# Kernel tuning notes

Hardware: AMD Instinct MI355X
Metric: run time of the kernel (lower is better)

The kernel has to match this reference:

```python
import jax, jax.numpy as jnp
import numpy as np

N = 262144
H = 256
POS_L, DIR_L = 10, 4


def _encode(x, L):
    # classic NeRF sinusoidal encoding with identity: [N,3] -> [N, 3 + 6*L]
    f = 2.0 ** jnp.arange(L, dtype=x.dtype)          # [L]
    xf = x[:, :, None] * f                            # [N,3,L]
    n = x.shape[0]
    return jnp.concatenate([x, jnp.sin(xf).reshape(n, -1), jnp.cos(xf).reshape(n, -1)], axis=1)


def setup_inputs() -> dict:
    key = jax.random.key(0)
    ks = iter(jax.random.split(key, 32))
    inp = {
        "pos": jax.random.normal(next(ks), (N, 3), jnp.float32),
        "dir": jax.random.normal(next(ks), (N, 3), jnp.float32),
        "pixel_width": jax.random.uniform(next(ks), (N, 1), dtype=jnp.float32),
        "t_start": jax.random.uniform(next(ks), (N, 1), dtype=jnp.float32),
        "t_end": jax.random.uniform(next(ks), (N, 1), dtype=jnp.float32),
    }
    pe_dim = 3 + 6 * POS_L   # 63
    de_dim = 3 + 6 * DIR_L   # 27
    dims = {
        "w00": (pe_dim, H), "w01": (H, H), "w02": (H, H), "w03": (H, H),
        "w10": (H + pe_dim, H), "w11": (H, H), "w12": (H, H), "w13": (H, H),
        "cw0": (H + de_dim, H // 2), "cw1": (H // 2, 4),
    }
    for name, (i, o) in dims.items():
        inp[name] = jax.random.normal(next(ks), (i, o), jnp.float32) * (1.0 / np.sqrt(i))
        inp[name.replace("w", "b", 1)] = jnp.zeros((o,), jnp.float32)
    return inp


def _nerf(pos, dir, w00, b00, w01, b01, w02, b02, w03, b03,
          w10, b10, w11, b11, w12, b12, w13, b13, cw0, cb0, cw1, cb1):
    pe = _encode(pos, POS_L)   # [N,63]
    de = _encode(dir, DIR_L)   # [N,27]
    r = jax.nn.relu
    # segment 0 (4 linears, ReLU between all, plus inter-segment ReLU)
    z = r(pe @ w00 + b00)
    z = r(z @ w01 + b01)
    z = r(z @ w02 + b02)
    z = r(z @ w03 + b03)
    # segment 1: positional encoding re-concatenated (skip connection)
    z = jnp.concatenate([z, pe], axis=1)              # [N,319]
    z = r(z @ w10 + b10)
    z = r(z @ w11 + b11)
    z = r(z @ w12 + b12)
    z = z @ w13 + b13                                 # no activation after last segment
    # color head: direction encoding concatenated (delayed_direction=True)
    h = r(jnp.concatenate([z, de], axis=1) @ cw0 + cb0)   # [N,128]
    out = h @ cw1 + cb1                                    # [N,4] (rgb + density, delayed_density=True)
    d = out[:, -1]
    density = jnp.where(d > 8.0, d, jax.nn.softplus(d))    # Softplus(threshold=8)
    rgb = jax.nn.sigmoid(out[:, :3])
    return density, rgb


def reference(pos, dir, pixel_width, t_start, t_end,
              w00, b00, w01, b01, w02, b02, w03, b03,
              w10, b10, w11, b11, w12, b12, w13, b13,
              cw0, cb0, cw1, cb1):
    # pixel_width / t_start / t_end are consumed only by mip-style encoders; the
    # classic sinusoidal encoder used here ignores them (kept for signature parity).
    return _nerf(pos, dir, w00, b00, w01, b01, w02, b02, w03, b03,
                 w10, b10, w11, b11, w12, b12, w13, b13, cw0, cb0, cw1, cb1)
```

## Files before the change

kernel.cpp:

```cpp
#include <hip/hip_runtime.h>
#include <hip/hip_bf16.h>
#include <math.h>

typedef unsigned short u16;
typedef unsigned int   u32;
typedef __bf16 bf16x8 __attribute__((ext_vector_type(8)));
typedef float  f32x4  __attribute__((ext_vector_type(4)));

#define NRAYS 262144
#define RPB   128
#define NBLK  (NRAYS / RPB)

enum : int { PO0=0, PO1=16384, PO2=81920, PO3=147456, PO4=212992,
             PO5=294912, PO6=360448, PO7=425984, PO8=491520, PO9=528384 };
#define TOTAL_PACK_ELEMS 530432

__device__ __forceinline__ u16 f2bf(float x) {
  return (u16)((__float_as_uint(x) + 0x8000u) >> 16);
}

struct PackArgs {
  const float* src[10];
  int K[10]; int N[10]; int l2mt[10]; int cstart[11];
};

__global__ __launch_bounds__(256) void pack_w(PackArgs a, u16* __restrict__ dst)
{
  int e = blockIdx.x * 256 + threadIdx.x;
  if (e >= TOTAL_PACK_ELEMS) return;
  int chunk = e >> 9;
  int li = 0;
  #pragma unroll
  for (int t = 1; t < 10; ++t) li += (chunk >= a.cstart[t]) ? 1 : 0;
  int lc = chunk - a.cstart[li];
  int ks = lc >> a.l2mt[li];
  int mt = lc - (ks << a.l2mt[li]);
  int lane = (e >> 3) & 63, j = e & 7;
  int k = ks * 32 + ((lane >> 4) << 3) + j;
  int n = mt * 16 + (lane & 15);
  float v = 0.f;
  if (k < a.K[li] && n < a.N[li]) v = a.src[li][(size_t)k * a.N[li] + n];
  u32 u = __float_as_uint(v);
  dst[e] = (u16)((u + 0x7FFFu + ((u >> 16) & 1u)) >> 16);
}

template<int MT_W>
__device__ __forceinline__ void binit(f32x4 acc[MT_W][4],
    const float* __restrict__ bias, int chbase, int lane)
{
  const int q = lane >> 4;
  #pragma unroll
  for (int mt = 0; mt < MT_W; ++mt) {
    float4 bv = *(const float4*)(bias + chbase + mt * 16 + q * 4);
    #pragma unroll
    for (int nt = 0; nt < 4; ++nt)
      acc[mt][nt] = (f32x4){bv.x, bv.y, bv.z, bv.w};
  }
}

template<int MT_W, int NSTEPS, int MT_TOTAL, int STRIDE>
__device__ __forceinline__ void gseg(f32x4 acc[MT_W][4],
    const u16* __restrict__ zb, int rhb, int cbase8,
    const u16* __restrict__ wl, int mt0, int ksbase, int lane)
{
  const int q = lane >> 4, llo = lane & 15;
  #pragma unroll
  for (int ks = 0; ks < NSTEPS; ++ks) {
    int c8s = ((cbase8 + ks * 4 + q) ^ (llo & 7));
    const u16* bp = zb + (rhb + llo) * STRIDE + c8s * 8;
    bf16x8 b[4];
    #pragma unroll
    for (int nt = 0; nt < 4; ++nt)
      b[nt] = *(const bf16x8*)(bp + nt * 16 * STRIDE);
    const u16* wp = wl + ((ksbase + ks) * MT_TOTAL + mt0) * 512 + lane * 8;
    bf16x8 a[MT_W];
    #pragma unroll
    for (int mt = 0; mt < MT_W; ++mt)
      a[mt] = *(const bf16x8*)(wp + mt * 512);
    #pragma unroll
    for (int mt = 0; mt < MT_W; ++mt)
      #pragma unroll
      for (int nt = 0; nt < 4; ++nt)
        acc[mt][nt] = __builtin_amdgcn_mfma_f32_16x16x32_bf16(a[mt], b[nt], acc[mt][nt], 0, 0, 0);
  }
}

template<int MT_W, bool RELU>
__device__ __forceinline__ void zstore(f32x4 acc[MT_W][4],
    int chbase, int rhb, u16* dst, int lane)
{
  const int llo = lane & 15, q = lane >> 4;
  #pragma unroll
  for (int mt = 0; mt < MT_W; ++mt) {
    int ch = chbase + mt * 16 + q * 4;
    int off0 = (((ch >> 3) ^ (llo & 7)) << 3) + (ch & 7);
    #pragma unroll
    for (int nt = 0; nt < 4; ++nt) {
      f32x4 v = acc[mt][nt];
      float x0 = v.x, x1 = v.y, x2 = v.z, x3 = v.w;
      if (RELU) { x0 = fmaxf(x0, 0.f); x1 = fmaxf(x1, 0.f);
                  x2 = fmaxf(x2, 0.f); x3 = fmaxf(x3, 0.f); }
      u32 a0 = __float_as_uint(x0) + 0x8000u;
      u32 a1 = __float_as_uint(x1) + 0x8000u;
      u32 a2 = __float_as_uint(x2) + 0x8000u;
      u32 a3 = __float_as_uint(x3) + 0x8000u;
      uint2 pk;
      pk.x = __builtin_amdgcn_perm(a1, a0, 0x07060302u);
      pk.y = __builtin_amdgcn_perm(a3, a2, 0x07060302u);
      *(uint2*)(dst + (rhb + nt * 16 + llo) * 256 + off0) = pk;
    }
  }
}

__device__ __forceinline__ void wr_pe(u16* peb, int r, int c, u16 v) {
  peb[r * 64 + (((c >> 3) ^ (r & 7)) << 3) + (c & 7)] = v;
}

__global__ __launch_bounds__(512, 4) void nerf_fused(
    const float* __restrict__ pos,  const float* __restrict__ dirv,
    const float* __restrict__ b00,  const float* __restrict__ b01,
    const float* __restrict__ b02,  const float* __restrict__ b03,
    const float* __restrict__ b10,  const float* __restrict__ b11,
    const float* __restrict__ b12,  const float* __restrict__ b13,
    const float* __restrict__ cb0,  const float* __restrict__ cb1,
    const u16* __restrict__ W, float* __restrict__ out)
{
  __shared__ __align__(16) u16 zb[RPB * 256];
  __shared__ __align__(16) u16 peb[RPB * 64];
  float* xyzf = (float*)zb;

  const int tid = threadIdx.x;
  const int rb  = blockIdx.x * RPB;
  const int lane = tid & 63, wid = tid >> 6;

  if (tid < 384) {
    int r = tid / 3, c = tid - r * 3;
    xyzf[r * 4 + c] = pos[(size_t)(rb + r) * 3 + c];
  }
  __syncthreads();

  #pragma unroll
  for (int i = tid; i < RPB * 30; i += 512) {
    int r = i / 30, t = i - r * 30;
    int j = t / 10, l = t - j * 10;
    float x = xyzf[r * 4 + j] * (float)(1 << l);
    wr_pe(peb, r, 3 + t,  f2bf(__sinf(x)));
    wr_pe(peb, r, 33 + t, f2bf(__cosf(x)));
  }
  {
    int r = tid >> 2, c = tid & 3;
    u16 v = 0; int col = 63;
    if (c < 3) { col = c; v = f2bf(xyzf[r * 4 + c]); }
    wr_pe(peb, r, col, v);
  }
  __syncthreads();

  f32x4 acc[4][4];
  const int mt0 = (wid & 3) * 4;
  const int chb = mt0 * 16;
  const int rh  = (wid >> 2) * 64;

  binit<4>(acc, b00, chb, lane);
  gseg<4, 2, 16, 64>(acc, peb, rh, 0, W + PO0, mt0, 0, lane);
  __syncthreads();
  zstore<4, true>(acc, chb, rh, zb, lane);
  __syncthreads();
  binit<4>(acc, b01, chb, lane);
  gseg<4, 8, 16, 256>(acc, zb, rh, 0, W + PO1, mt0, 0, lane);
  __syncthreads();
  zstore<4, true>(acc, chb, rh, zb, lane);
  __syncthreads();
  binit<4>(acc, b02, chb, lane);
  gseg<4, 8, 16, 256>(acc, zb, rh, 0, W + PO2, mt0, 0, lane);
  __syncthreads();
  zstore<4, true>(acc, chb, rh, zb, lane);
  __syncthreads();
  binit<4>(acc, b03, chb, lane);
  gseg<4, 8, 16, 256>(acc, zb, rh, 0, W + PO3, mt0, 0, lane);
  __syncthreads();
  zstore<4, true>(acc, chb, rh, zb, lane);
  __syncthreads();
  binit<4>(acc, b10, chb, lane);
  gseg<4, 8, 16, 256>(acc, zb, rh, 0, W + PO4, mt0, 0, lane);
  gseg<4, 2, 16, 64>(acc, peb, rh, 0, W + PO4, mt0, 8, lane);
  __syncthreads();
  zstore<4, true>(acc, chb, rh, zb, lane);
  #pragma unroll
  for (int i = tid; i < RPB * 16; i += 512) {
    int r = i >> 4, t = i & 15;
    if (t < 12) {
      int j = t >> 2, l = t & 3;
      float x = dirv[(size_t)(rb + r) * 3 + j] * (float)(1 << l);
      wr_pe(peb, r, 32 + 3 + t,  f2bf(__sinf(x)));
      wr_pe(peb, r, 32 + 15 + t, f2bf(__cosf(x)));
    } else {
      wr_pe(peb, r, 32 + 15 + t, 0);
    }
  }
  {
    int r = tid >> 2, c = tid & 3;
    u16 v = 0; int col = 31;
    if (c < 3) { col = c; v = f2bf(dirv[(size_t)(rb + r) * 3 + c]); }
    wr_pe(peb, r, 32 + col, v);
  }
  __syncthreads();
  binit<4>(acc, b11, chb, lane);
  gseg<4, 8, 16, 256>(acc, zb, rh, 0, W + PO5, mt0, 0, lane);
  __syncthreads();
  zstore<4, true>(acc, chb, rh, zb, lane);
  __syncthreads();
  binit<4>(acc, b12, chb, lane);
  gseg<4, 8, 16, 256>(acc, zb, rh, 0, W + PO6, mt0, 0, lane);
  __syncthreads();
  zstore<4, true>(acc, chb, rh, zb, lane);
  __syncthreads();
  binit<4>(acc, b13, chb, lane);
  gseg<4, 8, 16, 256>(acc, zb, rh, 0, W + PO7, mt0, 0, lane);
  __syncthreads();
  zstore<4, false>(acc, chb, rh, zb, lane);
  __syncthreads();
  {
    f32x4 acc8[2][4];
    const int m8 = (wid & 3) * 2;
    binit<2>(acc8, cb0, m8 * 16, lane);
    gseg<2, 8, 8, 256>(acc8, zb, rh, 0, W + PO8, m8, 0, lane);
    gseg<2, 1, 8, 64>(acc8, peb, rh, 4, W + PO8, m8, 8, lane);
    __syncthreads();
    zstore<2, true>(acc8, m8 * 16, rh, zb, lane);
    __syncthreads();
  }
  {
    const u16* W9 = W + PO9;
    const int q = lane >> 4, llo = lane & 15;
    const int r = wid * 16 + llo;
    f32x4 c9 = (f32x4){0.f, 0.f, 0.f, 0.f};
    #pragma unroll
    for (int ks = 0; ks < 4; ++ks) {
      int c8s = ((ks * 4 + q) ^ (llo & 7));
      bf16x8 b = *(const bf16x8*)(zb + r * 256 + c8s * 8);
      bf16x8 a = *(const bf16x8*)(W9 + ks * 512 + lane * 8);
      c9 = __builtin_amdgcn_mfma_f32_16x16x32_bf16(a, b, c9, 0, 0, 0);
    }
    if (q == 0) {
      int ray = rb + r;
      float o0 = c9.x + cb1[0];
      float o1 = c9.y + cb1[1];
      float o2 = c9.z + cb1[2];
      float dv = c9.w + cb1[3];
      out[ray] = (dv > 8.f) ? dv : log1pf(__expf(dv));
      float* rgb = out + NRAYS + (size_t)ray * 3;
      rgb[0] = 1.f / (1.f + __expf(-o0));
      rgb[1] = 1.f / (1.f + __expf(-o1));
      rgb[2] = 1.f / (1.f + __expf(-o2));
    }
  }
}

extern "C" void kernel_launch(void* const* d_in, const int* in_sizes, int n_in,
                              void* d_out, int out_size, void* d_ws, size_t ws_size,
                              hipStream_t stream)
{
  (void)in_sizes; (void)n_in; (void)out_size; (void)ws_size;
  const float* pos  = (const float*)d_in[0];
  const float* dirv = (const float*)d_in[1];
  PackArgs pa;
  const int widx[10] = {5, 7, 9, 11, 13, 15, 17, 19, 21, 23};
  const int K[10]    = {63, 256, 256, 256, 319, 256, 256, 256, 283, 128};
  const int Nn[10]   = {256, 256, 256, 256, 256, 256, 256, 256, 128, 4};
  const int L2MT[10] = {4, 4, 4, 4, 4, 4, 4, 4, 3, 0};
  const int CS[11]   = {0, 32, 160, 288, 416, 576, 704, 832, 960, 1032, 1036};
  for (int i = 0; i < 10; ++i) {
    pa.src[i] = (const float*)d_in[widx[i]];
    pa.K[i] = K[i]; pa.N[i] = Nn[i]; pa.l2mt[i] = L2MT[i];
  }
  for (int i = 0; i < 11; ++i) pa.cstart[i] = CS[i];

  u16* wp = (u16*)d_ws;
  hipLaunchKernelGGL(pack_w, dim3(TOTAL_PACK_ELEMS / 256), dim3(256), 0, stream, pa, wp);

  hipLaunchKernelGGL(nerf_fused, dim3(NBLK), dim3(512), 0, stream,
      pos, dirv,
      (const float*)d_in[6],  (const float*)d_in[8],
      (const float*)d_in[10], (const float*)d_in[12],
      (const float*)d_in[14], (const float*)d_in[16],
      (const float*)d_in[18], (const float*)d_in[20],
      (const float*)d_in[22], (const float*)d_in[24],
      wp, (float*)d_out);
}
```

Baseline: 391.3 us.

## Halve rays per block and stage direction encoding in a dedicated LDS buffer

```diff
diff --git a/kernel.cpp b/kernel.cpp
--- a/kernel.cpp
+++ b/kernel.cpp
@@ -8,7 +8,7 @@
 typedef float  f32x4  __attribute__((ext_vector_type(4)));
 
 #define NRAYS 262144
-#define RPB   128
+#define RPB   64
 #define NBLK  (NRAYS / RPB)
 
 enum : int { PO0=0, PO1=16384, PO2=81920, PO3=147456, PO4=212992,
@@ -44,8 +44,8 @@
   dst[e] = (u16)((u + 0x7FFFu + ((u >> 16) & 1u)) >> 16);
 }
 
-template<int MT_W>
-__device__ __forceinline__ void binit(f32x4 acc[MT_W][4],
+template<int MT_W, int NT>
+__device__ __forceinline__ void binit(f32x4 acc[MT_W][NT],
     const float* __restrict__ bias, int chbase, int lane)
 {
   const int q = lane >> 4;
@@ -53,24 +53,24 @@
   for (int mt = 0; mt < MT_W; ++mt) {
     float4 bv = *(const float4*)(bias + chbase + mt * 16 + q * 4);
     #pragma unroll
-    for (int nt = 0; nt < 4; ++nt)
+    for (int nt = 0; nt < NT; ++nt)
       acc[mt][nt] = (f32x4){bv.x, bv.y, bv.z, bv.w};
   }
 }
 
-template<int MT_W, int NSTEPS, int MT_TOTAL, int STRIDE>
-__device__ __forceinline__ void gseg(f32x4 acc[MT_W][4],
+template<int MT_W, int NT, int NSTEPS, int MT_TOTAL, int STRIDE, bool SWZ>
+__device__ __forceinline__ void gseg(f32x4 acc[MT_W][NT],
     const u16* __restrict__ zb, int rhb, int cbase8,
     const u16* __restrict__ wl, int mt0, int ksbase, int lane)
 {
   const int q = lane >> 4, llo = lane & 15;
   #pragma unroll
   for (int ks = 0; ks < NSTEPS; ++ks) {
-    int c8s = ((cbase8 + ks * 4 + q) ^ (llo & 7));
+    int c8s = (cbase8 + ks * 4 + q) ^ (SWZ ? (llo & 7) : 0);
     const u16* bp = zb + (rhb + llo) * STRIDE + c8s * 8;
-    bf16x8 b[4];
-    #pragma unroll
-    for (int nt = 0; nt < 4; ++nt)
+    bf16x8 b[NT];
+    #pragma unroll
+    for (int nt = 0; nt < NT; ++nt)
       b[nt] = *(const bf16x8*)(bp + nt * 16 * STRIDE);
     const u16* wp = wl + ((ksbase + ks) * MT_TOTAL + mt0) * 512 + lane * 8;
     bf16x8 a[MT_W];
@@ -80,13 +80,13 @@
     #pragma unroll
     for (int mt = 0; mt < MT_W; ++mt)
       #pragma unroll
-      for (int nt = 0; nt < 4; ++nt)
+      for (int nt = 0; nt < NT; ++nt)
         acc[mt][nt] = __builtin_amdgcn_mfma_f32_16x16x32_bf16(a[mt], b[nt], acc[mt][nt], 0, 0, 0);
   }
 }
 
-template<int MT_W, bool RELU>
-__device__ __forceinline__ void zstore(f32x4 acc[MT_W][4],
+template<int MT_W, int NT, bool RELU>
+__device__ __forceinline__ void zstore(f32x4 acc[MT_W][NT],
     int chbase, int rhb, u16* dst, int lane)
 {
   const int llo = lane & 15, q = lane >> 4;
@@ -95,7 +95,7 @@
     int ch = chbase + mt * 16 + q * 4;
     int off0 = (((ch >> 3) ^ (llo & 7)) << 3) + (ch & 7);
     #pragma unroll
-    for (int nt = 0; nt < 4; ++nt) {
+    for (int nt = 0; nt < NT; ++nt) {
       f32x4 v = acc[mt][nt];
       float x0 = v.x, x1 = v.y, x2 = v.z, x3 = v.w;
       if (RELU) { x0 = fmaxf(x0, 0.f); x1 = fmaxf(x1, 0.f);
@@ -127,15 +127,19 @@
 {
   __shared__ __align__(16) u16 zb[RPB * 256];
   __shared__ __align__(16) u16 peb[RPB * 64];
+  __shared__ __align__(16) u16 deb[RPB * 32];
   float* xyzf = (float*)zb;
 
   const int tid = threadIdx.x;
   const int rb  = blockIdx.x * RPB;
   const int lane = tid & 63, wid = tid >> 6;
 
-  if (tid < 384) {
+  if (tid < 192) {
     int r = tid / 3, c = tid - r * 3;
-    xyzf[r * 4 + c] = pos[(size_t)(rb + r) * 3 + c];
+    xyzf[r * 8 + c] = pos[(size_t)(rb + r) * 3 + c];
+  } else if (tid < 384) {
+    int t = tid - 192, r = t / 3, c = t - r * 3;
+    xyzf[r * 8 + 4 + c] = dirv[(size_t)(rb + r) * 3 + c];
   }
   __syncthreads();
 
@@ -143,93 +147,88 @@
   for (int i = tid; i < RPB * 30; i += 512) {
     int r = i / 30, t = i - r * 30;
     int j = t / 10, l = t - j * 10;
-    float x = xyzf[r * 4 + j] * (float)(1 << l);
+    float x = xyzf[r * 8 + j] * (float)(1 << l);
     wr_pe(peb, r, 3 + t,  f2bf(__sinf(x)));
     wr_pe(peb, r, 33 + t, f2bf(__cosf(x)));
   }
-  {
+  if (tid < 256) {
     int r = tid >> 2, c = tid & 3;
     u16 v = 0; int col = 63;
-    if (c < 3) { col = c; v = f2bf(xyzf[r * 4 + c]); }
+    if (c < 3) { col = c; v = f2bf(xyzf[r * 8 + c]); }
     wr_pe(peb, r, col, v);
   }
-  __syncthreads();
-
-  f32x4 acc[4][4];
+  #pragma unroll
+  for (int i = tid; i < RPB * 12; i += 512) {
+    int r = i / 12, t = i - r * 12;
+    int j = t >> 2, l = t & 3;
+    float x = xyzf[r * 8 + 4 + j] * (float)(1 << l);
+    deb[r * 32 + 3 + t]  = f2bf(__sinf(x));
+    deb[r * 32 + 15 + t] = f2bf(__cosf(x));
+  }
+  {
+    int r = tid >> 3, c = tid & 7;
+    u16 v = 0; int col = 24 + c;
+    if (c < 3) { col = c; v = f2bf(xyzf[r * 8 + 4 + c]); }
+    deb[r * 32 + col] = v;
+  }
+  __syncthreads();
+
+  f32x4 acc[4][2];
   const int mt0 = (wid & 3) * 4;
   const int chb = mt0 * 16;
-  const int rh  = (wid >> 2) * 64;
-
-  binit<4>(acc, b00, chb, lane);
-  gseg<4, 2, 16, 64>(acc, peb, rh, 0, W + PO0, mt0, 0, lane);
-  __syncthreads();
-  zstore<4, true>(acc, chb, rh, zb, lane);
-  __syncthreads();
-  binit<4>(acc, b01, chb, lane);
-  gseg<4, 8, 16, 256>(acc, zb, rh, 0, W + PO1, mt0, 0, lane);
-  __syncthreads();
-  zstore<4, true>(acc, chb, rh, zb, lane);
-  __syncthreads();
-  binit<4>(acc, b02, chb, lane);
-  gseg<4, 8, 16, 256>(acc, zb, rh, 0, W + PO2, mt0, 0, lane);
-  __syncthreads();
-  zstore<4, true>(acc, chb, rh, zb, lane);
-  __syncthreads();
-  binit<4>(acc, b03, chb, lane);
-  gseg<4, 8, 16, 256>(acc, zb, rh, 0, W + PO3, mt0, 0, lane);
-  __syncthreads();
-  zstore<4, true>(acc, chb, rh, zb, lane);
-  __syncthreads();
-  binit<4>(acc, b10, chb, lane);
-  gseg<4, 8, 16, 256>(acc, zb, rh, 0, W + PO4, mt0, 0, lane);
-  gseg<4, 2, 16, 64>(acc, peb, rh, 0, W + PO4, mt0, 8, lane);
-  __syncthreads();
-  zstore<4, true>(acc, chb, rh, zb, lane);
-  #pragma unroll
-  for (int i = tid; i < RPB * 16; i += 512) {
-    int r = i >> 4, t = i & 15;
-    if (t < 12) {
-      int j = t >> 2, l = t & 3;
-      float x = dirv[(size_t)(rb + r) * 3 + j] * (float)(1 << l);
-      wr_pe(peb, r, 32 + 3 + t,  f2bf(__sinf(x)));
-      wr_pe(peb, r, 32 + 15 + t, f2bf(__cosf(x)));
-    } else {
-      wr_pe(peb, r, 32 + 15 + t, 0);
-    }
-  }
+  const int rh  = (wid >> 2) * 32;
+
+  binit<4, 2>(acc, b00, chb, lane);
+  gseg<4, 2, 2, 16, 64, true>(acc, peb, rh, 0, W + PO0, mt0, 0, lane);
+  zstore<4, 2, true>(acc, chb, rh, zb, lane);
+  __syncthreads();
+  binit<4, 2>(acc, b01, chb, lane);
+  gseg<4, 2, 8, 16, 256, true>(acc, zb, rh, 0, W + PO1, mt0, 0, lane);
+  __syncthreads();
+  zstore<4, 2, true>(acc, chb, rh, zb, lane);
+  __syncthreads();
+  binit<4, 2>(acc, b02, chb, lane);
+  gseg<4, 2, 8, 16, 256, true>(acc, zb, rh, 0, W + PO2, mt0, 0, lane);
+  __syncthreads();
+  zstore<4, 2, true>(acc, chb, rh, zb, lane);
+  __syncthreads();
+  binit<4, 2>(acc, b03, chb, lane);
+  gseg<4, 2, 8, 16, 256, true>(acc, zb, rh, 0, W + PO3, mt0, 0, lane);
+  __syncthreads();
+  zstore<4, 2, true>(acc, chb, rh, zb, lane);
+  __syncthreads();
+  binit<4, 2>(acc, b10, chb, lane);
+  gseg<4, 2, 8, 16, 256, true>(acc, zb, rh, 0, W + PO4, mt0, 0, lane);
+  gseg<4, 2, 2, 16, 64, true>(acc, peb, rh, 0, W + PO4, mt0, 8, lane);
+  __syncthreads();
+  zstore<4, 2, true>(acc, chb, rh, zb, lane);
+  __syncthreads();
+  binit<4, 2>(acc, b11, chb, lane);
+  gseg<4, 2, 8, 16, 256, true>(acc, zb, rh, 0, W + PO5, mt0, 0, lane);
+  __syncthreads();
+  zstore<4, 2, true>(acc, chb, rh, zb, lane);
+  __syncthreads();
+  binit<4, 2>(acc, b12, chb, lane);
+  gseg<4, 2, 8, 16, 256, true>(acc, zb, rh, 0, W + PO6, mt0, 0, lane);
+  __syncthreads();
+  zstore<4, 2, true>(acc, chb, rh, zb, lane);
+  __syncthreads();
+  binit<4, 2>(acc, b13, chb, lane);
+  gseg<4, 2, 8, 16, 256, true>(acc, zb, rh, 0, W + PO7, mt0, 0, lane);
+  __syncthreads();
+  zstore<4, 2, false>(acc, chb, rh, zb, lane);
+  __syncthreads();
   {
-    int r = tid >> 2, c = tid & 3;
-    u16 v = 0; int col = 31;
-    if (c < 3) { col = c; v = f2bf(dirv[(size_t)(rb + r) * 3 + c]); }
-    wr_pe(peb, r, 32 + col, v);
-  }
-  __syncthreads();
-  binit<4>(acc, b11, chb, lane);
-  gseg<4, 8, 16, 256>(acc, zb, rh, 0, W + PO5, mt0, 0, lane);
-  __syncthreads();
-  zstore<4, true>(acc, chb, rh, zb, lane);
-  __syncthreads();
-  binit<4>(acc, b12, chb, lane);
-  gseg<4, 8, 16, 256>(acc, zb, rh, 0, W + PO6, mt0, 0, lane);
-  __syncthreads();
-  zstore<4, true>(acc, chb, rh, zb, lane);
-  __syncthreads();
-  binit<4>(acc, b13, chb, lane);
-  gseg<4, 8, 16, 256>(acc, zb, rh, 0, W + PO7, mt0, 0, lane);
-  __syncthreads();
-  zstore<4, false>(acc, chb, rh, zb, lane);
-  __syncthreads();
-  {
-    f32x4 acc8[2][4];
+    f32x4 acc8[2][2];
     const int m8 = (wid & 3) * 2;
-    binit<2>(acc8, cb0, m8 * 16, lane);
-    gseg<2, 8, 8, 256>(acc8, zb, rh, 0, W + PO8, m8, 0, lane);
-    gseg<2, 1, 8, 64>(acc8, peb, rh, 4, W + PO8, m8, 8, lane);
+    binit<2, 2>(acc8, cb0, m8 * 16, lane);
+    gseg<2, 2, 8, 8, 256, true>(acc8, zb, rh, 0, W + PO8, m8, 0, lane);
+    gseg<2, 2, 1, 8, 32, false>(acc8, deb, rh, 0, W + PO8, m8, 8, lane);
     __syncthreads();
-    zstore<2, true>(acc8, m8 * 16, rh, zb, lane);
+    zstore<2, 2, true>(acc8, m8 * 16, rh, zb, lane);
     __syncthreads();
   }
-  {
+  if (wid < 4) {
     const u16* W9 = W + PO9;
     const int q = lane >> 4, llo = lane & 15;
     const int r = wid * 16 + llo;
```

After: 434.5 us. 1.11x slower.
